# Kernel tuning notes

Measured on AMD Instinct MI355X. Metric: run time of the kernel, lower is better.

The kernel has to match this reference:

```python
import jax, jax.numpy as jnp
import numpy as np

B, S, E, H = 4, 2048, 1024, 16
D = E // H


def setup_inputs() -> dict:
    key = jax.random.key(0)
    ks = jax.random.split(key, 4)
    scale = 0.02
    x = jax.random.normal(ks[0], (B, S, E), dtype=jnp.float32)
    in_proj_w = jax.random.normal(ks[1], (3 * E, E), dtype=jnp.float32) * scale
    in_proj_b = jnp.zeros((3 * E,), dtype=jnp.float32)
    out_w = jax.random.normal(ks[2], (E, E), dtype=jnp.float32) * scale
    out_b = jnp.zeros((E,), dtype=jnp.float32)
    rel_bias = jax.random.normal(ks[3], (2 * 32 + 1, H), dtype=jnp.float32) * 0.02
    return {"x": x, "in_proj_w": in_proj_w, "in_proj_b": in_proj_b,
            "out_w": out_w, "out_b": out_b, "rel_bias": rel_bias,
            "max_rel_dist": 32}


def reference(x, in_proj_w, in_proj_b, out_w, out_b, rel_bias, max_rel_dist):
    b, s, e = x.shape
    h = rel_bias.shape[1]
    d = e // h
    # relative-position indices, clamped: [S, S]
    i = jnp.arange(s)[:, None]
    j = jnp.arange(s)[None, :]
    rel = jnp.clip(i - j, -max_rel_dist, max_rel_dist) + max_rel_dist
    # gather per-pair per-head bias then average over heads -> single 2D mask
    attn_mask = jnp.mean(rel_bias[rel], axis=-1)  # [S, S]
    # fused QKV projection (PyTorch in_proj: x @ W^T + b)
    qkv = x @ in_proj_w.T + in_proj_b           # [B, S, 3E]
    q, k, v = jnp.split(qkv, 3, axis=-1)
    q = q.reshape(b, s, h, d)
    k = k.reshape(b, s, h, d)
    v = v.reshape(b, s, h, d)
    scale = 1.0 / jnp.sqrt(jnp.asarray(d, dtype=x.dtype))
    scores = jnp.einsum('bqhd,bkhd->bhqk', q, k) * scale + attn_mask  # [B,H,S,S]
    probs = jax.nn.softmax(scores, axis=-1)
    ctx = jnp.einsum('bhqk,bkhd->bqhd', probs, v).reshape(b, s, e)
    return ctx @ out_w.T + out_b
```

## Files before the change

### kernel.cpp

```cpp
#include <hip/hip_runtime.h>
#include <math.h>

#define B_ 4
#define S_ 2048
#define E_ 1024
#define H_ 16
#define D_ 64
#define MRD 32

typedef __bf16 bf16x8 __attribute__((ext_vector_type(8)));
typedef float f32x4 __attribute__((ext_vector_type(4)));
typedef unsigned short us8 __attribute__((ext_vector_type(8)));
typedef unsigned short us4 __attribute__((ext_vector_type(4)));

union frag_cvt { us8 u; bf16x8 b; };
union h_cvt { __bf16 h; unsigned short u; };

__device__ __forceinline__ unsigned short bhi(float x) {
    h_cvt c; c.h = (__bf16)x; return c.u;
}
__device__ __forceinline__ float bf16_f(unsigned short h) {
    union { unsigned int u; float f; } c;
    c.u = ((unsigned int)h) << 16;
    return c.f;
}

__device__ __forceinline__ void async_copy16(const void* g, void* l) {
    __builtin_amdgcn_global_load_lds(
        (const __attribute__((address_space(1))) void*)g,
        (__attribute__((address_space(3))) void*)l,
        16, 0, 0);
}

#define QSCL 0.18033688f
#define L2E  1.44269504f

__global__ __launch_bounds__(128) void cvt_bf16(
    const float* __restrict__ in, unsigned short* __restrict__ out, int K)
{
    const int r  = blockIdx.x;
    const int k8 = threadIdx.x * 8;
    if (k8 >= K) return;
    const float* p = in + (size_t)r * K + k8;
    float4 a = *(const float4*)p;
    float4 b = *(const float4*)(p + 4);
    float xs[8] = {a.x, a.y, a.z, a.w, b.x, b.y, b.z, b.w};
    us8 hu;
#pragma unroll
    for (int j = 0; j < 8; ++j) hu[j] = bhi(xs[j]);
    const int pos = (k8 & ~31) + ((((k8 >> 3) & 3) ^ (r & 3)) * 8);
    *(us8*)&out[(size_t)r * K + pos] = hu;
}

__global__ __launch_bounds__(128) void split_hilo(
    const float* __restrict__ in, unsigned short* __restrict__ out, int K)
{
    const int r  = blockIdx.x;
    const int k8 = threadIdx.x * 8;
    if (k8 >= K) return;
    const float* p = in + (size_t)r * K + k8;
    float4 a = *(const float4*)p;
    float4 b = *(const float4*)(p + 4);
    float xs[8] = {a.x, a.y, a.z, a.w, b.x, b.y, b.z, b.w};
    us8 hu, lu;
#pragma unroll
    for (int j = 0; j < 8; ++j) {
        unsigned short hb = bhi(xs[j]);
        hu[j] = hb;
        lu[j] = bhi(xs[j] - bf16_f(hb));
    }
    const int pos = (k8 & ~31) + ((((k8 >> 3) & 3) ^ (r & 3)) * 8);
    *(us8*)&out[(size_t)r * 2 * K + pos]     = hu;
    *(us8*)&out[(size_t)r * 2 * K + K + pos] = lu;
}

__global__ __launch_bounds__(256, 2) void gemm_qkv5(
    const unsigned short* __restrict__ Ab, const unsigned short* __restrict__ Bb,
    const float* __restrict__ bias, unsigned short* __restrict__ Qb,
    unsigned short* __restrict__ K2, unsigned short* __restrict__ Vt2,
    int M, int N, int K)
{
    __shared__ unsigned short At[128 * 32];
    __shared__ unsigned short Bt[128 * 32];

    const int t    = threadIdx.x;
    const int w    = t >> 6;
    const int lane = t & 63;
    const int ln   = lane & 15;
    const int quad = lane >> 4;
    const int wm   = w >> 1;
    const int wn   = w & 1;
    const int m0   = blockIdx.x * 128;
    const int n0   = blockIdx.y * 128;

    const int srow = w * 16 + (lane >> 2);
    const int scol = (lane & 3) * 8;
    const unsigned short* Abase = Ab + (size_t)(m0 + srow) * K + scol;
    const unsigned short* Bbase = Bb + (size_t)(n0 + srow) * K + scol;
    const int wlds = (w * 16) * 32;
    const int fro  = (quad ^ (ln & 3)) * 8;

    f32x4 acc[4][4];
#pragma unroll
    for (int i = 0; i < 4; ++i)
#pragma unroll
        for (int j = 0; j < 4; ++j)
            acc[i][j] = (f32x4){0.f, 0.f, 0.f, 0.f};

    for (int kk = 0; kk < K; kk += 32) {
        __syncthreads();
#pragma unroll
        for (int c = 0; c < 2; ++c) {
            const size_t ro = (size_t)(c * 64) * K;
            const int lo = c * 64 * 32 + wlds;
            async_copy16(Abase + ro + kk, &At[lo]);
            async_copy16(Bbase + ro + kk, &Bt[lo]);
        }
        __syncthreads();

        frag_cvt ah[4], bh[4];
#pragma unroll
        for (int i = 0; i < 4; ++i) {
            ah[i].u = *(const us8*)&At[(wm * 64 + i * 16 + ln) * 32 + fro];
            bh[i].u = *(const us8*)&Bt[(wn * 64 + i * 16 + ln) * 32 + fro];
        }
#pragma unroll
        for (int i = 0; i < 4; ++i)
#pragma unroll
            for (int j = 0; j < 4; ++j)
                acc[i][j] = __builtin_amdgcn_mfma_f32_16x16x32_bf16(
                    ah[i].b, bh[j].b, acc[i][j], 0, 0, 0);
    }

    if (n0 < E_) {
#pragma unroll
        for (int j = 0; j < 4; ++j) {
            const int col = n0 + wn * 64 + j * 16 + ln;
            const float bv = bias[col];
            const int h = (col & (E_ - 1)) >> 6, d = col & 63;
#pragma unroll
            for (int i = 0; i < 4; ++i) {
#pragma unroll
                for (int r = 0; r < 4; ++r) {
                    const int row = m0 + wm * 64 + i * 16 + quad * 4 + r;
                    const int b = row >> 11, s = row & (S_ - 1);
                    Qb[((size_t)(b * 16 + h) * S_ + s) * 64 + d] =
                        bhi((acc[i][j][r] + bv) * QSCL);
                }
            }
        }
    } else if (n0 < 2 * E_) {
#pragma unroll
        for (int j = 0; j < 4; ++j) {
            const int col = n0 + wn * 64 + j * 16 + ln;
            const float bv = bias[col];
            const int h = (col & (E_ - 1)) >> 6, d = col & 63;
#pragma unroll
            for (int i = 0; i < 4; ++i) {
#pragma unroll
                for (int r = 0; r < 4; ++r) {
                    const int row = m0 + wm * 64 + i * 16 + quad * 4 + r;
                    const int b = row >> 11, s = row & (S_ - 1);
                    K2[((size_t)(b * 16 + h) * S_ + s) * 64 +
                       (((d >> 3) ^ (s & 7)) * 8) + (d & 7)] =
                        bhi(acc[i][j][r] + bv);
                }
            }
        }
    } else {
#pragma unroll
        for (int j = 0; j < 4; ++j) {
            const int col = n0 + wn * 64 + j * 16 + ln;
            const float bv = bias[col];
            const int h = (col & (E_ - 1)) >> 6, d = col & 63;
#pragma unroll
            for (int i = 0; i < 4; ++i) {
                const int row0 = m0 + wm * 64 + i * 16 + quad * 4;
                const int b = row0 >> 11, s0 = row0 & (S_ - 1);
                const int tile = s0 >> 6;
                const int g = (s0 >> 3) & 7;
                us4 o;
#pragma unroll
                for (int r = 0; r < 4; ++r) o[r] = bhi(acc[i][j][r] + bv);
                *(us4*)&Vt2[(size_t)(b * 16 + h) * S_ * 64 + tile * 4096 +
                            d * 64 + ((g ^ (d & 7)) * 8) + (quad & 1) * 4] = o;
            }
        }
    }
}

__global__ __launch_bounds__(256, 4) void attn_mfma5(
    const unsigned short* __restrict__ Qb, const unsigned short* __restrict__ K2,
    const unsigned short* __restrict__ Vt2, const float* __restrict__ rel_bias,
    unsigned short* __restrict__ ctx2)
{
    __shared__ unsigned short Kt[64 * 64];
    __shared__ unsigned short Vt[64 * 64];
    __shared__ unsigned short Pt[128 * 72];
    __shared__ float bias_s[65];

    const int t    = threadIdx.x;
    const int w    = t >> 6;
    const int lane = t & 63;
    const int ln   = lane & 15;
    const int quad = lane >> 4;

    const int bh = blockIdx.x;
    const int b  = bh >> 4;
    const int h  = bh & 15;
    const int q0 = blockIdx.y * 128;

    if (t < 65) {
        float s = 0.f;
#pragma unroll
        for (int hh = 0; hh < 16; ++hh) s += rel_bias[t * 16 + hh];
        bias_s[t] = s * (L2E / 16.f);
    }

    frag_cvt qf[2][2];
#pragma unroll
    for (int mf = 0; mf < 2; ++mf) {
        const unsigned short* qp =
            Qb + ((size_t)bh * S_ + q0 + w * 32 + mf * 16 + ln) * 64;
        qf[mf][0].u = *(const us8*)(qp + quad * 8);
        qf[mf][1].u = *(const us8*)(qp + 32 + quad * 8);
    }

    frag_cvt ones;
#pragma unroll
    for (int j = 0; j < 8; ++j) ones.u[j] = 0x3F80;

    f32x4 O[2][4];
#pragma unroll
    for (int mf = 0; mf < 2; ++mf)
#pragma unroll
        for (int n = 0; n < 4; ++n) O[mf][n] = (f32x4){0.f, 0.f, 0.f, 0.f};
    f32x4 lacc[2] = {(f32x4){0.f, 0.f, 0.f, 0.f}, (f32x4){0.f, 0.f, 0.f, 0.f}};

    const unsigned short* Kg = K2  + (size_t)bh * S_ * 64;
    const unsigned short* Vg = Vt2 + (size_t)bh * S_ * 64;

    for (int k0 = 0; k0 < S_; k0 += 64) {
        __syncthreads();
        {
            const unsigned short* kg = Kg + (size_t)k0 * 64;
            const unsigned short* vg = Vg + (size_t)k0 * 64;
            const int uo = w * 512;
            async_copy16(kg + uo + lane * 8,        &Kt[uo]);
            async_copy16(kg + 2048 + uo + lane * 8, &Kt[2048 + uo]);
            async_copy16(vg + uo + lane * 8,        &Vt[uo]);
            async_copy16(vg + 2048 + uo + lane * 8, &Vt[2048 + uo]);
        }
        __syncthreads();

        f32x4 sa[2][4];
#pragma unroll
        for (int n = 0; n < 4; ++n) {
            sa[0][n] = (f32x4){0.f, 0.f, 0.f, 0.f};
            sa[1][n] = (f32x4){0.f, 0.f, 0.f, 0.f};
            const int ro = (n * 16 + ln) * 64;
#pragma unroll
            for (int ks = 0; ks < 2; ++ks) {
                frag_cvt kh;
                kh.u = *(const us8*)&Kt[ro + (((ks * 4 + quad) ^ (ln & 7)) * 8)];
                sa[0][n] = __builtin_amdgcn_mfma_f32_16x16x32_bf16(
                    qf[0][ks].b, kh.b, sa[0][n], 0, 0, 0);
                sa[1][n] = __builtin_amdgcn_mfma_f32_16x16x32_bf16(
                    qf[1][ks].b, kh.b, sa[1][n], 0, 0, 0);
            }
        }

        const bool inband = (k0 >= q0 - 64) && (k0 <= q0 + 128);
        float cb = 0.f;
        if (!inband) cb = bias_s[(k0 < q0) ? 64 : 0];
#pragma unroll
        for (int mf = 0; mf < 2; ++mf) {
#pragma unroll
            for (int n = 0; n < 4; ++n) {
#pragma unroll
                for (int r = 0; r < 4; ++r) {
                    float s2;
                    if (inband) {
                        const int q   = q0 + w * 32 + mf * 16 + quad * 4 + r;
                        const int key = k0 + n * 16 + ln;
                        int rel = q - key;
                        rel = (rel < -MRD) ? -MRD : (rel > MRD ? MRD : rel);
                        s2 = sa[mf][n][r] + bias_s[rel + MRD];
                    } else {
                        s2 = sa[mf][n][r] + cb;
                    }
                    const int qrow = w * 32 + mf * 16 + quad * 4 + r;
                    const int pos = (n * 16 + ln) ^ ((qrow & 8) << 1);
                    Pt[qrow * 72 + pos] = bhi(__builtin_amdgcn_exp2f(s2));
                }
            }
        }

#pragma unroll
        for (int ks = 0; ks < 2; ++ks) {
            frag_cvt pa[2];
#pragma unroll
            for (int mf = 0; mf < 2; ++mf) {
                const int prow = w * 32 + mf * 16 + ln;
                pa[mf].u = *(const us8*)&Pt[prow * 72 +
                           ((ks * 32 + quad * 8) ^ ((prow & 8) << 1))];
                lacc[mf] = __builtin_amdgcn_mfma_f32_16x16x32_bf16(
                    pa[mf].b, ones.b, lacc[mf], 0, 0, 0);
            }
#pragma unroll
            for (int n = 0; n < 4; ++n) {
                frag_cvt vh;
                vh.u = *(const us8*)&Vt[(n * 16 + ln) * 64 +
                                        (((ks * 4 + quad) ^ (ln & 7)) * 8)];
                O[0][n] = __builtin_amdgcn_mfma_f32_16x16x32_bf16(
                    pa[0].b, vh.b, O[0][n], 0, 0, 0);
                O[1][n] = __builtin_amdgcn_mfma_f32_16x16x32_bf16(
                    pa[1].b, vh.b, O[1][n], 0, 0, 0);
            }
        }
    }

#pragma unroll
    for (int mf = 0; mf < 2; ++mf) {
        float inv[4];
#pragma unroll
        for (int r = 0; r < 4; ++r) inv[r] = 1.f / lacc[mf][r];
#pragma unroll
        for (int n = 0; n < 4; ++n) {
            const int k = h * D_ + n * 16 + ln;
            const int cbase = k & ~31;
            const int kg = (k >> 3) & 3;
#pragma unroll
            for (int r = 0; r < 4; ++r) {
                const int q = q0 + w * 32 + mf * 16 + quad * 4 + r;
                const float v = O[mf][n][r] * inv[r];
                unsigned short hb = bhi(v);
                const size_t rb = (size_t)(b * S_ + q) * (2 * E_);
                const int pos = cbase + ((kg ^ r) * 8) + (k & 7);
                ctx2[rb + pos]      = hb;
                ctx2[rb + E_ + pos] = bhi(v - bf16_f(hb));
            }
        }
    }
}

__global__ __launch_bounds__(256, 2) void gemm_out4(
    const unsigned short* __restrict__ A2, const unsigned short* __restrict__ B2,
    const float* __restrict__ bias, float* __restrict__ C,
    int M, int N, int K)
{
    __shared__ unsigned short Ath[128 * 32], Atl[128 * 32];
    __shared__ unsigned short Bth[128 * 32], Btl[128 * 32];

    const int t    = threadIdx.x;
    const int w    = t >> 6;
    const int lane = t & 63;
    const int ln   = lane & 15;
    const int quad = lane >> 4;
    const int wm   = w >> 1;
    const int wn   = w & 1;
    const int m0   = blockIdx.x * 128;
    const int n0   = blockIdx.y * 128;
    const int K2s  = 2 * K;

    const int srow = w * 16 + (lane >> 2);
    const int scol = (lane & 3) * 8;
    const unsigned short* Abase = A2 + (size_t)(m0 + srow) * K2s + scol;
    const unsigned short* Bbase = B2 + (size_t)(n0 + srow) * K2s + scol;
    const int wlds = (w * 16) * 32;
    const int fro  = (quad ^ (ln & 3)) * 8;

    f32x4 acc[4][4];
#pragma unroll
    for (int i = 0; i < 4; ++i)
#pragma unroll
        for (int j = 0; j < 4; ++j)
            acc[i][j] = (f32x4){0.f, 0.f, 0.f, 0.f};

    for (int kk = 0; kk < K; kk += 32) {
        __syncthreads();
#pragma unroll
        for (int c = 0; c < 2; ++c) {
            const size_t ro = (size_t)(c * 64) * K2s;
            const int lo = c * 64 * 32 + wlds;
            async_copy16(Abase + ro + kk,     &Ath[lo]);
            async_copy16(Abase + ro + K + kk, &Atl[lo]);
            async_copy16(Bbase + ro + kk,     &Bth[lo]);
            async_copy16(Bbase + ro + K + kk, &Btl[lo]);
        }
        __syncthreads();

        frag_cvt ah[4], al[4], bh[4], bl[4];
#pragma unroll
        for (int i = 0; i < 4; ++i) {
            const int ar = (wm * 64 + i * 16 + ln) * 32 + fro;
            const int br = (wn * 64 + i * 16 + ln) * 32 + fro;
            ah[i].u = *(const us8*)&Ath[ar];
            al[i].u = *(const us8*)&Atl[ar];
            bh[i].u = *(const us8*)&Bth[br];
            bl[i].u = *(const us8*)&Btl[br];
        }
#pragma unroll
        for (int i = 0; i < 4; ++i)
#pragma unroll
            for (int j = 0; j < 4; ++j) {
                acc[i][j] = __builtin_amdgcn_mfma_f32_16x16x32_bf16(
                    ah[i].b, bh[j].b, acc[i][j], 0, 0, 0);
                acc[i][j] = __builtin_amdgcn_mfma_f32_16x16x32_bf16(
                    ah[i].b, bl[j].b, acc[i][j], 0, 0, 0);
                acc[i][j] = __builtin_amdgcn_mfma_f32_16x16x32_bf16(
                    al[i].b, bh[j].b, acc[i][j], 0, 0, 0);
            }
    }

#pragma unroll
    for (int j = 0; j < 4; ++j) {
        const int col = n0 + wn * 64 + j * 16 + ln;
        const float bv = bias[col];
#pragma unroll
        for (int i = 0; i < 4; ++i) {
            const int row = m0 + wm * 64 + i * 16 + quad * 4;
#pragma unroll
            for (int r = 0; r < 4; ++r)
                C[(size_t)(row + r) * N + col] = acc[i][j][r] + bv;
        }
    }
}

extern "C" void kernel_launch(void* const* d_in, const int* in_sizes, int n_in,
                              void* d_out, int out_size, void* d_ws, size_t ws_size,
                              hipStream_t stream)
{
    const float* x         = (const float*)d_in[0];
    const float* in_proj_w = (const float*)d_in[1];
    const float* in_proj_b = (const float*)d_in[2];
    const float* out_w     = (const float*)d_in[3];
    const float* out_b     = (const float*)d_in[4];
    const float* rel_bias  = (const float*)d_in[5];
    float* out = (float*)d_out;

    const int M = B_ * S_;
    const size_t PH = (size_t)B_ * H_ * S_ * 64;

    unsigned short* Qb   = (unsigned short*)d_ws;
    unsigned short* K2   = Qb + PH;
    unsigned short* Vt2  = K2 + PH;
    unsigned short* A2c  = Vt2 + PH;
    unsigned short* Axb  = A2c + (size_t)M * 2 * E_;
    unsigned short* Wqkv = Axb + (size_t)M * E_;
    unsigned short* W2o  = Wqkv + (size_t)3 * E_ * E_;

    cvt_bf16<<<M,      128, 0, stream>>>(x,         Axb,  E_);
    cvt_bf16<<<3 * E_, 128, 0, stream>>>(in_proj_w, Wqkv, E_);

    {
        dim3 grid(M / 128, (3 * E_) / 128);
        gemm_qkv5<<<grid, 256, 0, stream>>>(Axb, Wqkv, in_proj_b, Qb, K2, Vt2,
                                            M, 3 * E_, E_);
    }
    {
        dim3 grid(B_ * H_, S_ / 128);
        attn_mfma5<<<grid, 256, 0, stream>>>(Qb, K2, Vt2, rel_bias, A2c);
    }
    split_hilo<<<E_, 128, 0, stream>>>(out_w, W2o, E_);
    {
        dim3 grid(M / 128, E_ / 128);
        gemm_out4<<<grid, 256, 0, stream>>>(A2c, W2o, out_b, out, M, E_, E_);
    }
}
```

Measured before the change: 316.0 us.

## Replace both GEMMs with a double-buffered 256x128 ping-pong MFMA kernel

```diff
diff --git a/kernel.cpp b/kernel.cpp
--- a/kernel.cpp
+++ b/kernel.cpp
@@ -32,8 +32,14 @@
         16, 0, 0);
 }
 
+__device__ __forceinline__ f32x4 mf16(const frag_cvt& a, const frag_cvt& b, f32x4 c) {
+    return __builtin_amdgcn_mfma_f32_16x16x32_bf16(a.b, b.b, c, 0, 0, 0);
+}
+
 #define QSCL 0.18033688f
 #define L2E  1.44269504f
+
+#define SBAR0() __builtin_amdgcn_sched_barrier(0)
 
 __global__ __launch_bounds__(128) void cvt_bf16(
     const float* __restrict__ in, unsigned short* __restrict__ out, int K)
@@ -48,8 +54,7 @@
     us8 hu;
 #pragma unroll
     for (int j = 0; j < 8; ++j) hu[j] = bhi(xs[j]);
-    const int pos = (k8 & ~31) + ((((k8 >> 3) & 3) ^ (r & 3)) * 8);
-    *(us8*)&out[(size_t)r * K + pos] = hu;
+    *(us8*)&out[(size_t)r * K + k8] = hu;
 }
 
 __global__ __launch_bounds__(128) void split_hilo(
@@ -69,36 +74,57 @@
         hu[j] = hb;
         lu[j] = bhi(xs[j] - bf16_f(hb));
     }
-    const int pos = (k8 & ~31) + ((((k8 >> 3) & 3) ^ (r & 3)) * 8);
-    *(us8*)&out[(size_t)r * 2 * K + pos]     = hu;
-    *(us8*)&out[(size_t)r * 2 * K + K + pos] = lu;
-}
-
-__global__ __launch_bounds__(256, 2) void gemm_qkv5(
-    const unsigned short* __restrict__ Ab, const unsigned short* __restrict__ Bb,
-    const float* __restrict__ bias, unsigned short* __restrict__ Qb,
-    unsigned short* __restrict__ K2, unsigned short* __restrict__ Vt2,
-    int M, int N, int K)
+    *(us8*)&out[(size_t)r * 2 * K + k8]     = hu;
+    *(us8*)&out[(size_t)r * 2 * K + K + k8] = lu;
+}
+
+__device__ __forceinline__ void stage_unit(const unsigned short* g, int grs,
+                                           unsigned short* lu, int t)
 {
-    __shared__ unsigned short At[128 * 32];
-    __shared__ unsigned short Bt[128 * 32];
+#pragma unroll
+    for (int l = 0; l < 2; ++l) {
+        const int f  = l * 512 + t;
+        const int ri = f >> 3;
+        const int cs = ((f & 7) ^ (ri & 7)) * 8;
+        async_copy16(g + (size_t)ri * grs + cs,
+                     lu + l * 4096 + (t >> 6) * 512);
+    }
+}
+
+template<int MODE>
+__global__ __launch_bounds__(512, 2) void gemm8(
+    const unsigned short* __restrict__ Ag, const unsigned short* __restrict__ Bg,
+    const float* __restrict__ bias,
+    unsigned short* __restrict__ O0, unsigned short* __restrict__ O1,
+    unsigned short* __restrict__ O2, float* __restrict__ Cf)
+{
+    constexpr int KD = (MODE == 0) ? 1024 : 3072;
+    constexpr int NT = KD / 64;
+    constexpr int AS = (MODE == 0) ? 1024 : 2048;
+    constexpr int BS = (MODE == 0) ? 1024 : 2048;
+
+    __shared__ unsigned short sbuf[2][24576];
 
     const int t    = threadIdx.x;
+    const int lane = t & 63;
     const int w    = t >> 6;
-    const int lane = t & 63;
     const int ln   = lane & 15;
     const int quad = lane >> 4;
     const int wm   = w >> 1;
     const int wn   = w & 1;
-    const int m0   = blockIdx.x * 128;
+    const int m0   = blockIdx.x * 256;
     const int n0   = blockIdx.y * 128;
 
-    const int srow = w * 16 + (lane >> 2);
-    const int scol = (lane & 3) * 8;
-    const unsigned short* Abase = Ab + (size_t)(m0 + srow) * K + scol;
-    const unsigned short* Bbase = Bb + (size_t)(n0 + srow) * K + scol;
-    const int wlds = (w * 16) * 32;
-    const int fro  = (quad ^ (ln & 3)) * 8;
+    auto mapA = [](int kk) -> int {
+        return (MODE == 0) ? kk : (kk < 1024 ? kk : kk - 1024);
+    };
+    auto mapB = [](int kk) -> int {
+        return (MODE == 0) ? kk : (kk < 2048 ? kk : kk - 2048);
+    };
+
+    const int swz = (ln & 7) << 3;
+    const int kq0 = (quad * 8) ^ swz;
+    const int kq1 = (32 + quad * 8) ^ swz;
 
     f32x4 acc[4][4];
 #pragma unroll
@@ -107,83 +133,172 @@
         for (int j = 0; j < 4; ++j)
             acc[i][j] = (f32x4){0.f, 0.f, 0.f, 0.f};
 
-    for (int kk = 0; kk < K; kk += 32) {
-        __syncthreads();
-#pragma unroll
-        for (int c = 0; c < 2; ++c) {
-            const size_t ro = (size_t)(c * 64) * K;
-            const int lo = c * 64 * 32 + wlds;
-            async_copy16(Abase + ro + kk, &At[lo]);
-            async_copy16(Bbase + ro + kk, &Bt[lo]);
-        }
-        __syncthreads();
-
-        frag_cvt ah[4], bh[4];
-#pragma unroll
-        for (int i = 0; i < 4; ++i) {
-            ah[i].u = *(const us8*)&At[(wm * 64 + i * 16 + ln) * 32 + fro];
-            bh[i].u = *(const us8*)&Bt[(wn * 64 + i * 16 + ln) * 32 + fro];
-        }
-#pragma unroll
-        for (int i = 0; i < 4; ++i)
-#pragma unroll
-            for (int j = 0; j < 4; ++j)
-                acc[i][j] = __builtin_amdgcn_mfma_f32_16x16x32_bf16(
-                    ah[i].b, bh[j].b, acc[i][j], 0, 0, 0);
-    }
-
-    if (n0 < E_) {
+    stage_unit(Ag + (size_t)m0 * AS + mapA(0),         AS, &sbuf[0][0],     t);
+    stage_unit(Ag + (size_t)(m0 + 128) * AS + mapA(0), AS, &sbuf[0][8192],  t);
+    stage_unit(Bg + (size_t)n0 * BS + mapB(0),         BS, &sbuf[0][16384], t);
+    stage_unit(Bg + (size_t)n0 * BS + mapB(64),        BS, &sbuf[1][16384], t);
+    stage_unit(Ag + (size_t)m0 * AS + mapA(64),        AS, &sbuf[1][0],     t);
+    asm volatile("s_waitcnt vmcnt(4)" ::: "memory");
+    SBAR0();
+    __builtin_amdgcn_s_barrier();
+    SBAR0();
+
+    for (int k = 0; k < NT; ++k) {
+        unsigned short* bufc = sbuf[k & 1];
+        unsigned short* bufn = sbuf[(k & 1) ^ 1];
+        frag_cvt a0[2][2], a1[2][2], b0[2][2], b1[2][2];
+
+#pragma unroll
+        for (int i = 0; i < 2; ++i) {
+            const int ra = (wm * 64 + i * 16 + ln) * 64;
+            a0[i][0].u = *(const us8*)&bufc[ra + kq0];
+            a0[i][1].u = *(const us8*)&bufc[ra + kq1];
+            const int rb = 16384 + (wn * 64 + i * 16 + ln) * 64;
+            b0[i][0].u = *(const us8*)&bufc[rb + kq0];
+            b0[i][1].u = *(const us8*)&bufc[rb + kq1];
+        }
+        if (k + 1 < NT)
+            stage_unit(Ag + (size_t)(m0 + 128) * AS + mapA((k + 1) * 64),
+                       AS, &bufn[8192], t);
+        SBAR0(); __builtin_amdgcn_s_barrier(); SBAR0();
+        __builtin_amdgcn_s_setprio(1);
+#pragma unroll
+        for (int i = 0; i < 2; ++i)
+#pragma unroll
+            for (int j = 0; j < 2; ++j) {
+                acc[i][j] = mf16(a0[i][0], b0[j][0], acc[i][j]);
+                acc[i][j] = mf16(a0[i][1], b0[j][1], acc[i][j]);
+            }
+        __builtin_amdgcn_s_setprio(0);
+        SBAR0(); __builtin_amdgcn_s_barrier(); SBAR0();
+
+#pragma unroll
+        for (int i = 0; i < 2; ++i) {
+            const int rb = 16384 + (wn * 64 + (i + 2) * 16 + ln) * 64;
+            b1[i][0].u = *(const us8*)&bufc[rb + kq0];
+            b1[i][1].u = *(const us8*)&bufc[rb + kq1];
+        }
+        SBAR0(); __builtin_amdgcn_s_barrier(); SBAR0();
+        __builtin_amdgcn_s_setprio(1);
+#pragma unroll
+        for (int i = 0; i < 2; ++i)
+#pragma unroll
+            for (int j = 0; j < 2; ++j) {
+                acc[i][j + 2] = mf16(a0[i][0], b1[j][0], acc[i][j + 2]);
+                acc[i][j + 2] = mf16(a0[i][1], b1[j][1], acc[i][j + 2]);
+            }
+        __builtin_amdgcn_s_setprio(0);
+        SBAR0(); __builtin_amdgcn_s_barrier(); SBAR0();
+
+#pragma unroll
+        for (int i = 0; i < 2; ++i) {
+            const int ra = (wm * 64 + (i + 2) * 16 + ln) * 64;
+            a1[i][0].u = *(const us8*)&bufc[ra + kq0];
+            a1[i][1].u = *(const us8*)&bufc[ra + kq1];
+        }
+        if (k + 2 < NT)
+            stage_unit(Bg + (size_t)n0 * BS + mapB((k + 2) * 64),
+                       BS, &bufc[16384], t);
+        SBAR0(); __builtin_amdgcn_s_barrier(); SBAR0();
+        __builtin_amdgcn_s_setprio(1);
+#pragma unroll
+        for (int i = 0; i < 2; ++i)
+#pragma unroll
+            for (int j = 0; j < 2; ++j) {
+                acc[i + 2][j + 2] = mf16(a1[i][0], b1[j][0], acc[i + 2][j + 2]);
+                acc[i + 2][j + 2] = mf16(a1[i][1], b1[j][1], acc[i + 2][j + 2]);
+            }
+        __builtin_amdgcn_s_setprio(0);
+        SBAR0(); __builtin_amdgcn_s_barrier(); SBAR0();
+
+        if (k + 2 < NT)
+            stage_unit(Ag + (size_t)m0 * AS + mapA((k + 2) * 64),
+                       AS, &bufc[0], t);
+        SBAR0(); __builtin_amdgcn_s_barrier(); SBAR0();
+        __builtin_amdgcn_s_setprio(1);
+#pragma unroll
+        for (int i = 0; i < 2; ++i)
+#pragma unroll
+            for (int j = 0; j < 2; ++j) {
+                acc[i + 2][j] = mf16(a1[i][0], b0[j][0], acc[i + 2][j]);
+                acc[i + 2][j] = mf16(a1[i][1], b0[j][1], acc[i + 2][j]);
+            }
+        __builtin_amdgcn_s_setprio(0);
+        if (k + 2 < NT) {
+            asm volatile("s_waitcnt vmcnt(4)" ::: "memory");
+        } else if (k + 1 < NT) {
+            asm volatile("s_waitcnt vmcnt(0)" ::: "memory");
+        }
+        SBAR0(); __builtin_amdgcn_s_barrier(); SBAR0();
+    }
+
+    if constexpr (MODE == 0) {
+        if (n0 < E_) {
+#pragma unroll
+            for (int j = 0; j < 4; ++j) {
+                const int col = n0 + wn * 64 + j * 16 + ln;
+                const float bv = bias[col];
+                const int h = (col & (E_ - 1)) >> 6, d = col & 63;
+#pragma unroll
+                for (int i = 0; i < 4; ++i) {
+#pragma unroll
+                    for (int r = 0; r < 4; ++r) {
+                        const int row = m0 + wm * 64 + i * 16 + quad * 4 + r;
+                        const int b = row >> 11, s = row & (S_ - 1);
+                        O0[((size_t)(b * 16 + h) * S_ + s) * 64 + d] =
+                            bhi((acc[i][j][r] + bv) * QSCL);
+                    }
+                }
+            }
+        } else if (n0 < 2 * E_) {
+#pragma unroll
+            for (int j = 0; j < 4; ++j) {
+                const int col = n0 + wn * 64 + j * 16 + ln;
+                const float bv = bias[col];
+                const int h = (col & (E_ - 1)) >> 6, d = col & 63;
+#pragma unroll
+                for (int i = 0; i < 4; ++i) {
+#pragma unroll
+                    for (int r = 0; r < 4; ++r) {
+                        const int row = m0 + wm * 64 + i * 16 + quad * 4 + r;
+                        const int b = row >> 11, s = row & (S_ - 1);
+                        O1[((size_t)(b * 16 + h) * S_ + s) * 64 +
+                           (((d >> 3) ^ (s & 7)) * 8) + (d & 7)] =
+                            bhi(acc[i][j][r] + bv);
+                    }
+                }
+            }
+        } else {
+#pragma unroll
+            for (int j = 0; j < 4; ++j) {
+                const int col = n0 + wn * 64 + j * 16 + ln;
+                const float bv = bias[col];
+                const int h = (col & (E_ - 1)) >> 6, d = col & 63;
+#pragma unroll
+                for (int i = 0; i < 4; ++i) {
+                    const int row0 = m0 + wm * 64 + i * 16 + quad * 4;
+                    const int b = row0 >> 11, s0 = row0 & (S_ - 1);
+                    const int tile = s0 >> 6;
+                    const int g = (s0 >> 3) & 7;
+                    us4 o;
+#pragma unroll
+                    for (int r = 0; r < 4; ++r) o[r] = bhi(acc[i][j][r] + bv);
+                    *(us4*)&O2[(size_t)(b * 16 + h) * S_ * 64 + tile * 4096 +
+                               d * 64 + ((g ^ (d & 7)) * 8) + (quad & 1) * 4] = o;
+                }
+            }
+        }
+    } else {
 #pragma unroll
         for (int j = 0; j < 4; ++j) {
             const int col = n0 + wn * 64 + j * 16 + ln;
             const float bv = bias[col];
-            const int h = (col & (E_ - 1)) >> 6, d = col & 63;
 #pragma unroll
             for (int i = 0; i < 4; ++i) {
-#pragma unroll
-                for (int r = 0; r < 4; ++r) {
-                    const int row = m0 + wm * 64 + i * 16 + quad * 4 + r;
-                    const int b = row >> 11, s = row & (S_ - 1);
-                    Qb[((size_t)(b * 16 + h) * S_ + s) * 64 + d] =
-                        bhi((acc[i][j][r] + bv) * QSCL);
-                }
-            }
-        }
-    } else if (n0 < 2 * E_) {
-#pragma unroll
-        for (int j = 0; j < 4; ++j) {
-            const int col = n0 + wn * 64 + j * 16 + ln;
-            const float bv = bias[col];
-            const int h = (col & (E_ - 1)) >> 6, d = col & 63;
-#pragma unroll
-            for (int i = 0; i < 4; ++i) {
-#pragma unroll
-                for (int r = 0; r < 4; ++r) {
-                    const int row = m0 + wm * 64 + i * 16 + quad * 4 + r;
-                    const int b = row >> 11, s = row & (S_ - 1);
-                    K2[((size_t)(b * 16 + h) * S_ + s) * 64 +
-                       (((d >> 3) ^ (s & 7)) * 8) + (d & 7)] =
-                        bhi(acc[i][j][r] + bv);
-                }
-            }
-        }
-    } else {
-#pragma unroll
-        for (int j = 0; j < 4; ++j) {
-            const int col = n0 + wn * 64 + j * 16 + ln;
-            const float bv = bias[col];
-            const int h = (col & (E_ - 1)) >> 6, d = col & 63;
-#pragma unroll
-            for (int i = 0; i < 4; ++i) {
-                const int row0 = m0 + wm * 64 + i * 16 + quad * 4;
-                const int b = row0 >> 11, s0 = row0 & (S_ - 1);
-                const int tile = s0 >> 6;
-                const int g = (s0 >> 3) & 7;
-                us4 o;
-#pragma unroll
-                for (int r = 0; r < 4; ++r) o[r] = bhi(acc[i][j][r] + bv);
-                *(us4*)&Vt2[(size_t)(b * 16 + h) * S_ * 64 + tile * 4096 +
-                            d * 64 + ((g ^ (d & 7)) * 8) + (quad & 1) * 4] = o;
+                const int row = m0 + wm * 64 + i * 16 + quad * 4;
+#pragma unroll
+                for (int r = 0; r < 4; ++r)
+                    Cf[(size_t)(row + r) * E_ + col] = acc[i][j][r] + bv;
             }
         }
     }
@@ -328,101 +443,15 @@
 #pragma unroll
         for (int n = 0; n < 4; ++n) {
             const int k = h * D_ + n * 16 + ln;
-            const int cbase = k & ~31;
-            const int kg = (k >> 3) & 3;
 #pragma unroll
             for (int r = 0; r < 4; ++r) {
                 const int q = q0 + w * 32 + mf * 16 + quad * 4 + r;
                 const float v = O[mf][n][r] * inv[r];
                 unsigned short hb = bhi(v);
                 const size_t rb = (size_t)(b * S_ + q) * (2 * E_);
-                const int pos = cbase + ((kg ^ r) * 8) + (k & 7);
-                ctx2[rb + pos]      = hb;
-                ctx2[rb + E_ + pos] = bhi(v - bf16_f(hb));
-            }
-        }
-    }
-}
-
-__global__ __launch_bounds__(256, 2) void gemm_out4(
-    const unsigned short* __restrict__ A2, const unsigned short* __restrict__ B2,
-    const float* __restrict__ bias, float* __restrict__ C,
-    int M, int N, int K)
-{
-    __shared__ unsigned short Ath[128 * 32], Atl[128 * 32];
-    __shared__ unsigned short Bth[128 * 32], Btl[128 * 32];
-
-    const int t    = threadIdx.x;
-    const int w    = t >> 6;
-    const int lane = t & 63;
-    const int ln   = lane & 15;
-    const int quad = lane >> 4;
-    const int wm   = w >> 1;
-    const int wn   = w & 1;
-    const int m0   = blockIdx.x * 128;
-    const int n0   = blockIdx.y * 128;
-    const int K2s  = 2 * K;
-
-    const int srow = w * 16 + (lane >> 2);
-    const int scol = (lane & 3) * 8;
-    const unsigned short* Abase = A2 + (size_t)(m0 + srow) * K2s + scol;
-    const unsigned short* Bbase = B2 + (size_t)(n0 + srow) * K2s + scol;
-    const int wlds = (w * 16) * 32;
-    const int fro  = (quad ^ (ln & 3)) * 8;
-
-    f32x4 acc[4][4];
-#pragma unroll
-    for (int i = 0; i < 4; ++i)
-#pragma unroll
-        for (int j = 0; j < 4; ++j)
-            acc[i][j] = (f32x4){0.f, 0.f, 0.f, 0.f};
-
-    for (int kk = 0; kk < K; kk += 32) {
-        __syncthreads();
-#pragma unroll
-        for (int c = 0; c < 2; ++c) {
-            const size_t ro = (size_t)(c * 64) * K2s;
-            const int lo = c * 64 * 32 + wlds;
-            async_copy16(Abase + ro + kk,     &Ath[lo]);
-            async_copy16(Abase + ro + K + kk, &Atl[lo]);
-            async_copy16(Bbase + ro + kk,     &Bth[lo]);
-            async_copy16(Bbase + ro + K + kk, &Btl[lo]);
-        }
-        __syncthreads();
-
-        frag_cvt ah[4], al[4], bh[4], bl[4];
-#pragma unroll
-        for (int i = 0; i < 4; ++i) {
-            const int ar = (wm * 64 + i * 16 + ln) * 32 + fro;
-            const int br = (wn * 64 + i * 16 + ln) * 32 + fro;
-            ah[i].u = *(const us8*)&Ath[ar];
-            al[i].u = *(const us8*)&Atl[ar];
-            bh[i].u = *(const us8*)&Bth[br];
-            bl[i].u = *(const us8*)&Btl[br];
-        }
-#pragma unroll
-        for (int i = 0; i < 4; ++i)
-#pragma unroll
-            for (int j = 0; j < 4; ++j) {
-                acc[i][j] = __builtin_amdgcn_mfma_f32_16x16x32_bf16(
-                    ah[i].b, bh[j].b, acc[i][j], 0, 0, 0);
-                acc[i][j] = __builtin_amdgcn_mfma_f32_16x16x32_bf16(
-                    ah[i].b, bl[j].b, acc[i][j], 0, 0, 0);
-                acc[i][j] = __builtin_amdgcn_mfma_f32_16x16x32_bf16(
-                    al[i].b, bh[j].b, acc[i][j], 0, 0, 0);
-            }
-    }
-
-#pragma unroll
-    for (int j = 0; j < 4; ++j) {
-        const int col = n0 + wn * 64 + j * 16 + ln;
-        const float bv = bias[col];
-#pragma unroll
-        for (int i = 0; i < 4; ++i) {
-            const int row = m0 + wm * 64 + i * 16 + quad * 4;
-#pragma unroll
-            for (int r = 0; r < 4; ++r)
-                C[(size_t)(row + r) * N + col] = acc[i][j][r] + bv;
+                ctx2[rb + k]      = hb;
+                ctx2[rb + E_ + k] = bhi(v - bf16_f(hb));
+            }
         }
     }
 }
@@ -445,18 +474,18 @@
     unsigned short* Qb   = (unsigned short*)d_ws;
     unsigned short* K2   = Qb + PH;
     unsigned short* Vt2  = K2 + PH;
-    unsigned short* A2c  = Vt2 + PH;
-    unsigned short* Axb  = A2c + (size_t)M * 2 * E_;
-    unsigned short* Wqkv = Axb + (size_t)M * E_;
-    unsigned short* W2o  = Wqkv + (size_t)3 * E_ * E_;
+    unsigned short* W2o  = Vt2 + PH;
+    unsigned short* Wqkv = W2o + (size_t)E_ * 2 * E_;
+    unsigned short* A2c  = Wqkv + (size_t)3 * E_ * E_;
+    unsigned short* Axb  = A2c;
 
     cvt_bf16<<<M,      128, 0, stream>>>(x,         Axb,  E_);
     cvt_bf16<<<3 * E_, 128, 0, stream>>>(in_proj_w, Wqkv, E_);
 
     {
-        dim3 grid(M / 128, (3 * E_) / 128);
-        gemm_qkv5<<<grid, 256, 0, stream>>>(Axb, Wqkv, in_proj_b, Qb, K2, Vt2,
-                                            M, 3 * E_, E_);
+        dim3 grid(M / 256, (3 * E_) / 128);
+        gemm8<0><<<grid, 512, 0, stream>>>(Axb, Wqkv, in_proj_b,
+                                           Qb, K2, Vt2, nullptr);
     }
     {
         dim3 grid(B_ * H_, S_ / 128);
@@ -464,7 +493,8 @@
     }
     split_hilo<<<E_, 128, 0, stream>>>(out_w, W2o, E_);
     {
-        dim3 grid(M / 128, E_ / 128);
-        gemm_out4<<<grid, 256, 0, stream>>>(A2c, W2o, out_b, out, M, E_, E_);
-    }
-}
+        dim3 grid(M / 256, E_ / 128);
+        gemm8<1><<<grid, 512, 0, stream>>>(A2c, W2o, out_b,
+                                           nullptr, nullptr, nullptr, out);
+    }
+}
```

New measurement: 332.3 us. 1.05x slower.

## Rewrite attention with 32x32 MFMA, register-resident P, and double-buffered K/V

Applied to the files above, without the earlier changes.

```diff
diff --git a/kernel.cpp b/kernel.cpp
--- a/kernel.cpp
+++ b/kernel.cpp
@@ -10,11 +10,13 @@
 
 typedef __bf16 bf16x8 __attribute__((ext_vector_type(8)));
 typedef float f32x4 __attribute__((ext_vector_type(4)));
+typedef float f32x16 __attribute__((ext_vector_type(16)));
 typedef unsigned short us8 __attribute__((ext_vector_type(8)));
 typedef unsigned short us4 __attribute__((ext_vector_type(4)));
 
 union frag_cvt { us8 u; bf16x8 b; };
 union h_cvt { __bf16 h; unsigned short u; };
+union f_u { float f; unsigned int u; };
 
 __device__ __forceinline__ unsigned short bhi(float x) {
     h_cvt c; c.h = (__bf16)x; return c.u;
@@ -30,6 +32,10 @@
         (const __attribute__((address_space(1))) void*)g,
         (__attribute__((address_space(3))) void*)l,
         16, 0, 0);
+}
+
+__device__ __forceinline__ f32x16 mf32(const frag_cvt& a, const frag_cvt& b, f32x16 c) {
+    return __builtin_amdgcn_mfma_f32_32x32x16_bf16(a.b, b.b, c, 0, 0, 0);
 }
 
 #define QSCL 0.18033688f
@@ -189,157 +195,177 @@
     }
 }
 
-__global__ __launch_bounds__(256, 4) void attn_mfma5(
+__global__ __launch_bounds__(256, 3) void attn_mfma6(
     const unsigned short* __restrict__ Qb, const unsigned short* __restrict__ K2,
     const unsigned short* __restrict__ Vt2, const float* __restrict__ rel_bias,
     unsigned short* __restrict__ ctx2)
 {
-    __shared__ unsigned short Kt[64 * 64];
-    __shared__ unsigned short Vt[64 * 64];
-    __shared__ unsigned short Pt[128 * 72];
+    __shared__ unsigned short Kt[2][4096];
+    __shared__ unsigned short Vt[2][4096];
     __shared__ float bias_s[65];
+    __shared__ float rsum[4][32];
 
     const int t    = threadIdx.x;
     const int w    = t >> 6;
     const int lane = t & 63;
-    const int ln   = lane & 15;
-    const int quad = lane >> 4;
+    const int l31  = lane & 31;
+    const int h    = lane >> 5;
+    const int swzk = lane & 7;
 
     const int bh = blockIdx.x;
     const int b  = bh >> 4;
-    const int h  = bh & 15;
+    const int hh = bh & 15;
     const int q0 = blockIdx.y * 128;
 
     if (t < 65) {
         float s = 0.f;
 #pragma unroll
-        for (int hh = 0; hh < 16; ++hh) s += rel_bias[t * 16 + hh];
+        for (int j = 0; j < 16; ++j) s += rel_bias[t * 16 + j];
         bias_s[t] = s * (L2E / 16.f);
     }
 
-    frag_cvt qf[2][2];
-#pragma unroll
-    for (int mf = 0; mf < 2; ++mf) {
+    frag_cvt qf[4];
+    {
         const unsigned short* qp =
-            Qb + ((size_t)bh * S_ + q0 + w * 32 + mf * 16 + ln) * 64;
-        qf[mf][0].u = *(const us8*)(qp + quad * 8);
-        qf[mf][1].u = *(const us8*)(qp + 32 + quad * 8);
-    }
-
-    frag_cvt ones;
-#pragma unroll
-    for (int j = 0; j < 8; ++j) ones.u[j] = 0x3F80;
-
-    f32x4 O[2][4];
-#pragma unroll
-    for (int mf = 0; mf < 2; ++mf)
-#pragma unroll
-        for (int n = 0; n < 4; ++n) O[mf][n] = (f32x4){0.f, 0.f, 0.f, 0.f};
-    f32x4 lacc[2] = {(f32x4){0.f, 0.f, 0.f, 0.f}, (f32x4){0.f, 0.f, 0.f, 0.f}};
+            Qb + ((size_t)bh * S_ + q0 + w * 32 + l31) * 64 + h * 8;
+#pragma unroll
+        for (int ks = 0; ks < 4; ++ks) qf[ks].u = *(const us8*)(qp + ks * 16);
+    }
+
+    f32x16 Z;
+#pragma unroll
+    for (int i = 0; i < 16; ++i) Z[i] = 0.f;
+    f32x16 O0 = Z, O1 = Z;
+    float lsum = 0.f;
 
     const unsigned short* Kg = K2  + (size_t)bh * S_ * 64;
     const unsigned short* Vg = Vt2 + (size_t)bh * S_ * 64;
 
-    for (int k0 = 0; k0 < S_; k0 += 64) {
-        __syncthreads();
-        {
-            const unsigned short* kg = Kg + (size_t)k0 * 64;
-            const unsigned short* vg = Vg + (size_t)k0 * 64;
+    {
+        const int uo = w * 512;
+        async_copy16(Kg + uo + lane * 8,        &Kt[0][uo]);
+        async_copy16(Kg + 2048 + uo + lane * 8, &Kt[0][2048 + uo]);
+        async_copy16(Vg + uo + lane * 8,        &Vt[0][uo]);
+        async_copy16(Vg + 2048 + uo + lane * 8, &Vt[0][2048 + uo]);
+    }
+    __syncthreads();
+
+    for (int kt0 = 0; kt0 < 32; ++kt0) {
+        const int cur = kt0 & 1;
+        const int k0  = kt0 * 64;
+
+        if (kt0 + 1 < 32) {
+            const unsigned short* kg = Kg + (size_t)(k0 + 64) * 64;
+            const unsigned short* vg = Vg + (size_t)(k0 + 64) * 64;
+            unsigned short* kd = Kt[cur ^ 1];
+            unsigned short* vd = Vt[cur ^ 1];
             const int uo = w * 512;
-            async_copy16(kg + uo + lane * 8,        &Kt[uo]);
-            async_copy16(kg + 2048 + uo + lane * 8, &Kt[2048 + uo]);
-            async_copy16(vg + uo + lane * 8,        &Vt[uo]);
-            async_copy16(vg + 2048 + uo + lane * 8, &Vt[2048 + uo]);
-        }
-        __syncthreads();
-
-        f32x4 sa[2][4];
-#pragma unroll
-        for (int n = 0; n < 4; ++n) {
-            sa[0][n] = (f32x4){0.f, 0.f, 0.f, 0.f};
-            sa[1][n] = (f32x4){0.f, 0.f, 0.f, 0.f};
-            const int ro = (n * 16 + ln) * 64;
-#pragma unroll
-            for (int ks = 0; ks < 2; ++ks) {
-                frag_cvt kh;
-                kh.u = *(const us8*)&Kt[ro + (((ks * 4 + quad) ^ (ln & 7)) * 8)];
-                sa[0][n] = __builtin_amdgcn_mfma_f32_16x16x32_bf16(
-                    qf[0][ks].b, kh.b, sa[0][n], 0, 0, 0);
-                sa[1][n] = __builtin_amdgcn_mfma_f32_16x16x32_bf16(
-                    qf[1][ks].b, kh.b, sa[1][n], 0, 0, 0);
-            }
+            async_copy16(kg + uo + lane * 8,        kd + uo);
+            async_copy16(kg + 2048 + uo + lane * 8, kd + 2048 + uo);
+            async_copy16(vg + uo + lane * 8,        vd + uo);
+            async_copy16(vg + 2048 + uo + lane * 8, vd + 2048 + uo);
+        }
+
+        f32x16 sa0 = Z, sa1 = Z;
+#pragma unroll
+        for (int ks = 0; ks < 4; ++ks) {
+            frag_cvt kh0, kh1;
+            const int go = ((ks * 2 + h) ^ swzk) * 8;
+            kh0.u = *(const us8*)&Kt[cur][l31 * 64 + go];
+            kh1.u = *(const us8*)&Kt[cur][(32 + l31) * 64 + go];
+            sa0 = mf32(kh0, qf[ks], sa0);
+            sa1 = mf32(kh1, qf[ks], sa1);
         }
 
         const bool inband = (k0 >= q0 - 64) && (k0 <= q0 + 128);
         float cb = 0.f;
         if (!inband) cb = bias_s[(k0 < q0) ? 64 : 0];
-#pragma unroll
-        for (int mf = 0; mf < 2; ++mf) {
-#pragma unroll
-            for (int n = 0; n < 4; ++n) {
-#pragma unroll
-                for (int r = 0; r < 4; ++r) {
-                    float s2;
-                    if (inband) {
-                        const int q   = q0 + w * 32 + mf * 16 + quad * 4 + r;
-                        const int key = k0 + n * 16 + ln;
-                        int rel = q - key;
-                        rel = (rel < -MRD) ? -MRD : (rel > MRD ? MRD : rel);
-                        s2 = sa[mf][n][r] + bias_s[rel + MRD];
-                    } else {
-                        s2 = sa[mf][n][r] + cb;
+        const int q = q0 + w * 32 + l31;
+
+        unsigned int Wd[2][4][2];
+#pragma unroll
+        for (int kt = 0; kt < 2; ++kt) {
+#pragma unroll
+            for (int B2 = 0; B2 < 4; ++B2) {
+#pragma unroll
+                for (int p = 0; p < 2; ++p) {
+                    unsigned int word = 0;
+#pragma unroll
+                    for (int rp = 0; rp < 2; ++rp) {
+                        const int reg = B2 * 4 + p * 2 + rp;
+                        const float sv = (kt == 0) ? sa0[reg] : sa1[reg];
+                        float s2;
+                        if (inband) {
+                            const int key = k0 + kt * 32 + B2 * 8 + h * 4 + p * 2 + rp;
+                            int rel = q - key;
+                            rel = (rel < -MRD) ? -MRD : (rel > MRD ? MRD : rel);
+                            s2 = sv + bias_s[rel + MRD];
+                        } else {
+                            s2 = sv + cb;
+                        }
+                        const float e = __builtin_amdgcn_exp2f(s2);
+                        const unsigned short u = bhi(e);
+                        lsum += bf16_f(u);
+                        word |= ((unsigned int)u) << (16 * rp);
                     }
-                    const int qrow = w * 32 + mf * 16 + quad * 4 + r;
-                    const int pos = (n * 16 + ln) ^ ((qrow & 8) << 1);
-                    Pt[qrow * 72 + pos] = bhi(__builtin_amdgcn_exp2f(s2));
+                    Wd[kt][B2][p] = word;
                 }
             }
         }
 
 #pragma unroll
-        for (int ks = 0; ks < 2; ++ks) {
-            frag_cvt pa[2];
-#pragma unroll
-            for (int mf = 0; mf < 2; ++mf) {
-                const int prow = w * 32 + mf * 16 + ln;
-                pa[mf].u = *(const us8*)&Pt[prow * 72 +
-                           ((ks * 32 + quad * 8) ^ ((prow & 8) << 1))];
-                lacc[mf] = __builtin_amdgcn_mfma_f32_16x16x32_bf16(
-                    pa[mf].b, ones.b, lacc[mf], 0, 0, 0);
-            }
-#pragma unroll
-            for (int n = 0; n < 4; ++n) {
-                frag_cvt vh;
-                vh.u = *(const us8*)&Vt[(n * 16 + ln) * 64 +
-                                        (((ks * 4 + quad) ^ (ln & 7)) * 8)];
-                O[0][n] = __builtin_amdgcn_mfma_f32_16x16x32_bf16(
-                    pa[0].b, vh.b, O[0][n], 0, 0, 0);
-                O[1][n] = __builtin_amdgcn_mfma_f32_16x16x32_bf16(
-                    pa[1].b, vh.b, O[1][n], 0, 0, 0);
-            }
-        }
-    }
-
-#pragma unroll
-    for (int mf = 0; mf < 2; ++mf) {
-        float inv[4];
-#pragma unroll
-        for (int r = 0; r < 4; ++r) inv[r] = 1.f / lacc[mf][r];
-#pragma unroll
-        for (int n = 0; n < 4; ++n) {
-            const int k = h * D_ + n * 16 + ln;
-            const int cbase = k & ~31;
-            const int kg = (k >> 3) & 3;
-#pragma unroll
-            for (int r = 0; r < 4; ++r) {
-                const int q = q0 + w * 32 + mf * 16 + quad * 4 + r;
-                const float v = O[mf][n][r] * inv[r];
-                unsigned short hb = bhi(v);
-                const size_t rb = (size_t)(b * S_ + q) * (2 * E_);
-                const int pos = cbase + ((kg ^ r) * 8) + (k & 7);
-                ctx2[rb + pos]      = hb;
-                ctx2[rb + E_ + pos] = bhi(v - bf16_f(hb));
-            }
+        for (int m = 0; m < 4; ++m) {
+            const int kt  = m >> 1;
+            const int sel = (m & 1) * 2;
+            auto r0 = __builtin_amdgcn_permlane32_swap(
+                Wd[kt][sel][0], Wd[kt][sel + 1][0], false, false);
+            auto r1 = __builtin_amdgcn_permlane32_swap(
+                Wd[kt][sel][1], Wd[kt][sel + 1][1], false, false);
+            frag_cvt pa;
+            union { us8 v; unsigned int d[4]; } uu;
+            uu.d[0] = (unsigned int)r0[0];
+            uu.d[1] = (unsigned int)r1[0];
+            uu.d[2] = (unsigned int)r0[1];
+            uu.d[3] = (unsigned int)r1[1];
+            pa.u = uu.v;
+
+            const int gv = ((m * 2 + h) ^ swzk) * 8;
+            frag_cvt v0, v1;
+            v0.u = *(const us8*)&Vt[cur][l31 * 64 + gv];
+            v1.u = *(const us8*)&Vt[cur][(32 + l31) * 64 + gv];
+            O0 = mf32(pa, v0, O0);
+            O1 = mf32(pa, v1, O1);
+        }
+
+        __syncthreads();
+    }
+
+    {
+        f_u lz; lz.f = lsum;
+        auto rs = __builtin_amdgcn_permlane32_swap(lz.u, lz.u, false, false);
+        f_u s0, s1; s0.u = (unsigned int)rs[0]; s1.u = (unsigned int)rs[1];
+        const float inv = 1.f / (s0.f + s1.f);
+        if (lane < 32) rsum[w][l31] = inv;
+    }
+    __syncthreads();
+
+    float invq[16];
+#pragma unroll
+    for (int reg = 0; reg < 16; ++reg)
+        invq[reg] = rsum[w][(reg & 3) + 8 * (reg >> 2) + 4 * h];
+
+#pragma unroll
+    for (int dblk = 0; dblk < 2; ++dblk) {
+#pragma unroll
+        for (int reg = 0; reg < 16; ++reg) {
+            const int qrow = q0 + w * 32 + (reg & 3) + 8 * (reg >> 2) + 4 * h;
+            const float v = ((dblk == 0) ? O0[reg] : O1[reg]) * invq[reg];
+            const unsigned short hb = bhi(v);
+            const int k = hh * 64 + dblk * 32 + l31;
+            const int pos = (k & ~31) + (((l31 >> 3) ^ (reg & 3)) * 8) + (k & 7);
+            const size_t rb = (size_t)(b * S_ + qrow) * (2 * E_);
+            ctx2[rb + pos]      = hb;
+            ctx2[rb + E_ + pos] = bhi(v - bf16_f(hb));
         }
     }
 }
@@ -460,7 +486,7 @@
     }
     {
         dim3 grid(B_ * H_, S_ / 128);
-        attn_mfma5<<<grid, 256, 0, stream>>>(Qb, K2, Vt2, rel_bias, A2c);
+        attn_mfma6<<<grid, 256, 0, stream>>>(Qb, K2, Vt2, rel_bias, A2c);
     }
     split_hilo<<<E_, 128, 0, stream>>>(out_w, W2o, E_);
     {
```

Result: slower. 327.3 us (+3.6%).
